# Optimization experiments

Measured on AMD Instinct MI355X. Metric: run time of the kernel, lower is better.

The kernel has to match this reference:

```python
import jax, jax.numpy as jnp
import numpy as np

N_A, N_P = 100000, 150000
N = N_A + N_P          # total nodes in concatenated feature matrix
D = 128                # emb_dim == hidden
C = 16                 # num_classes
E = 2000000            # nnz per relation


def setup_inputs() -> dict:
    key = jax.random.key(0)
    ks = jax.random.split(key, 16)
    s = 1.0 / np.sqrt(D)
    # coefficients as in init_coe: uniform(-b, b) then L1-normalized, coe_num = 1+2+2 = 5
    bound = np.sqrt(3.0 / 5)
    coe_np = np.random.RandomState(0).uniform(-bound, bound, 5)
    coe_np = coe_np / np.sum(np.abs(coe_np))
    return {
        "x0": jax.random.normal(ks[0], (N_A, D), jnp.float32),
        "x1": jax.random.normal(ks[1], (N_P, D), jnp.float32),
        "vals_ap": jax.random.uniform(ks[2], (E,), jnp.float32) * 0.01,
        "vals_pa": jax.random.uniform(ks[3], (E,), jnp.float32) * 0.01,
        # AP: rows are A nodes [0, N_A), cols are P nodes [N_A, N)
        "rows_ap": jax.random.randint(ks[4], (E,), 0, N_A, jnp.int32),
        "cols_ap": jax.random.randint(ks[5], (E,), N_A, N, jnp.int32),
        # PA: rows are P nodes [N_A, N), cols are A nodes [0, N_A)
        "rows_pa": jax.random.randint(ks[6], (E,), N_A, N, jnp.int32),
        "cols_pa": jax.random.randint(ks[7], (E,), 0, N_A, jnp.int32),
        "Wp0": jax.random.normal(ks[8], (D, D), jnp.float32) * s,
        "Wp1": jax.random.normal(ks[9], (D, D), jnp.float32) * s,
        "W1": jax.random.normal(ks[10], (D, D), jnp.float32) * s,
        "b1": jnp.zeros((D,), jnp.float32),
        "W2": jax.random.normal(ks[11], (D, C), jnp.float32) * s,
        "b2": jnp.zeros((C,), jnp.float32),
        "coe": jnp.asarray(coe_np, jnp.float32),
    }


def _spmm(rows, cols, vals, h):
    # sparse [N,N] @ dense [N,D] via gather + segment-sum
    return jax.ops.segment_sum(vals[:, None] * h[cols], rows, num_segments=N)


def _normalize(x):
    mean = x.mean(axis=1, keepdims=True)
    std = jnp.std(x, axis=1, keepdims=True, ddof=1)  # torch std is unbiased
    z = (x - mean) / std
    return jnp.where(jnp.isnan(z), 0.0, z)


def _power_pass(x, coe, ap, pa, first_order):
    # first_order: tuple of relation names in hop-1 order ("AP","PA") or ("PA","AP")
    rel = {"AP": ap, "PA": pa}
    res = coe[0] * x
    h = {}
    for ci, r in enumerate(first_order):
        h[r] = _spmm(*rel[r], x)
        res = res + coe[1 + ci] * h[r]
    # hop 2: compose relation j[:2] with previous result j[2:]
    second = [r + first_order[1 - i] for i, r in enumerate(first_order)]
    for ci, j in enumerate(second):
        out = _spmm(*rel[j[:2]], h[j[2:]])
        res = res + coe[3 + ci] * out
    return res


def reference(x0, x1, vals_ap, vals_pa, rows_ap, cols_ap, rows_pa, cols_pa,
              Wp0, Wp1, W1, b1, W2, b2, coe):
    ap = (rows_ap, cols_ap, vals_ap)
    pa = (rows_pa, cols_pa, vals_pa)
    # per-type projection then concat along node axis
    x = jnp.concatenate([x0 @ Wp0, x1 @ Wp1], axis=0)  # [N, D]
    x = jax.nn.relu(x @ W1 + b1)
    x = _normalize(x)
    # pass 1: lis = {1: [AP, PA], 2: [APPA, PAAP]}
    x = _power_pass(x, coe, ap, pa, ("AP", "PA"))
    # pass 2 (transposed series): lis_t = {1: [PA, AP], 2: [PAAP, APPA]}
    res = _power_pass(x, coe, ap, pa, ("PA", "AP"))
    return res @ W2 + b2  # [N, C]
```

## Files before the change

### kernel.cpp

```cpp
#include <hip/hip_runtime.h>
#include <hip/hip_bf16.h>


typedef float f32x2 __attribute__((ext_vector_type(2)));
typedef float f32x4 __attribute__((ext_vector_type(4)));
typedef short bf16x8 __attribute__((ext_vector_type(8)));

__device__ inline unsigned short f2bf(float x) {
    unsigned b = __float_as_uint(x);
    unsigned r = (b + 0x7fffu + ((b >> 16) & 1u)) >> 16;
    return (unsigned short)r;
}
__device__ inline float bflo(unsigned u) { return __uint_as_float(u << 16); }
__device__ inline float bfhi(unsigned u) { return __uint_as_float(u & 0xffff0000u); }

__device__ inline unsigned pk_fp8x4(float a, float b, float c, float d) {
    int v = __builtin_amdgcn_cvt_pk_fp8_f32(a, b, 0, false);
    v = __builtin_amdgcn_cvt_pk_fp8_f32(c, d, v, true);
    return (unsigned)v;
}

__global__ __launch_bounds__(128) void fuse_w(const float* __restrict__ Wp0,
                                              const float* __restrict__ Wp1,
                                              const float* __restrict__ W1,
                                              unsigned short* __restrict__ Mt0,
                                              unsigned short* __restrict__ Mt1) {
    int m = blockIdx.x >> 7;
    int i = blockIdx.x & 127;
    const float* Wp = m ? Wp1 : Wp0;
    unsigned short* Mt = m ? Mt1 : Mt0;
    __shared__ float r[128];
    int t = threadIdx.x;
    r[t] = Wp[i * 128 + t];
    __syncthreads();
    float acc = 0.f;
    #pragma unroll 8
    for (int k = 0; k < 128; ++k) acc += r[k] * W1[k * 128 + t];
    Mt[t * 128 + i] = f2bf(acc);
}

__global__ __launch_bounds__(256) void gemm_relu_norm(const float* __restrict__ xin,
                                                      const unsigned short* __restrict__ Mt,
                                                      const float* __restrict__ b1,
                                                      unsigned short* __restrict__ xbf,
                                                      unsigned char* __restrict__ x8,
                                                      int nrows) {
    __shared__ char xsh[64 * 256];
    __shared__ char xsl[64 * 256];
    __shared__ char mts[128 * 256];
    int t = threadIdx.x;
    long row0 = (long)blockIdx.x * 64;
    int rows_this = nrows - (int)row0;
    if (rows_this > 64) rows_this = 64;

    #pragma unroll
    for (int it = 0; it < 4; ++it) {
        int idx = it * 256 + t;
        int row = idx >> 4, slot = idx & 15;
        float4 v0 = {0.f, 0.f, 0.f, 0.f}, v1 = {0.f, 0.f, 0.f, 0.f};
        if (row < rows_this) {
            v0 = *(const float4*)(xin + (row0 + row) * 128 + slot * 8);
            v1 = *(const float4*)(xin + (row0 + row) * 128 + slot * 8 + 4);
        }
        float vv[8] = {v0.x, v0.y, v0.z, v0.w, v1.x, v1.y, v1.z, v1.w};
        unsigned hw[8], lw[8];
        #pragma unroll
        for (int j = 0; j < 8; ++j) {
            unsigned h = f2bf(vv[j]);
            float hv = __uint_as_float(h << 16);
            hw[j] = h;
            lw[j] = f2bf(vv[j] - hv);
        }
        uint4 ph, pl;
        ph.x = hw[0] | (hw[1] << 16); ph.y = hw[2] | (hw[3] << 16);
        ph.z = hw[4] | (hw[5] << 16); ph.w = hw[6] | (hw[7] << 16);
        pl.x = lw[0] | (lw[1] << 16); pl.y = lw[2] | (lw[3] << 16);
        pl.z = lw[4] | (lw[5] << 16); pl.w = lw[6] | (lw[7] << 16);
        int off = row * 256 + ((slot ^ (row & 7)) << 4);
        *(uint4*)&xsh[off] = ph;
        *(uint4*)&xsl[off] = pl;
    }
    #pragma unroll
    for (int it = 0; it < 8; ++it) {
        int idx = it * 256 + t;
        int row = idx >> 4, slot = idx & 15;
        uint4 mv = ((const uint4*)Mt)[idx];
        *(uint4*)&mts[row * 256 + ((slot ^ (row & 7)) << 4)] = mv;
    }
    __syncthreads();

    int w = t >> 6;
    int lidx = t & 15;
    int grp = (t >> 4) & 3;
    f32x4 acc[8];
    #pragma unroll
    for (int nt = 0; nt < 8; ++nt) acc[nt] = (f32x4){0.f, 0.f, 0.f, 0.f};

    #pragma unroll
    for (int ks = 0; ks < 4; ++ks) {
        int arow = w * 16 + lidx;
        int slot = ks * 4 + grp;
        bf16x8 ah = *(bf16x8*)&xsh[arow * 256 + ((slot ^ (arow & 7)) << 4)];
        bf16x8 al = *(bf16x8*)&xsl[arow * 256 + ((slot ^ (arow & 7)) << 4)];
        #pragma unroll
        for (int nt = 0; nt < 8; ++nt) {
            int brow = nt * 16 + lidx;
            bf16x8 bb = *(bf16x8*)&mts[brow * 256 + ((slot ^ (brow & 7)) << 4)];
            acc[nt] = __builtin_amdgcn_mfma_f32_16x16x32_bf16(al, bb, acc[nt], 0, 0, 0);
            acc[nt] = __builtin_amdgcn_mfma_f32_16x16x32_bf16(ah, bb, acc[nt], 0, 0, 0);
        }
    }

    float bias[8];
    #pragma unroll
    for (int nt = 0; nt < 8; ++nt) bias[nt] = b1[nt * 16 + lidx];

    #pragma unroll
    for (int r = 0; r < 4; ++r) {
        int row_loc = w * 16 + grp * 4 + r;
        float v[8];
        float s = 0.f;
        #pragma unroll
        for (int nt = 0; nt < 8; ++nt) {
            float x = acc[nt][r] + bias[nt];
            x = x > 0.f ? x : 0.f;
            v[nt] = x;
            s += x;
        }
        s += __shfl_xor(s, 1); s += __shfl_xor(s, 2);
        s += __shfl_xor(s, 4); s += __shfl_xor(s, 8);
        float mean = s * (1.0f / 128.0f);
        float q = 0.f;
        #pragma unroll
        for (int nt = 0; nt < 8; ++nt) {
            float d = v[nt] - mean;
            v[nt] = d;
            q += d * d;
        }
        q += __shfl_xor(q, 1); q += __shfl_xor(q, 2);
        q += __shfl_xor(q, 4); q += __shfl_xor(q, 8);
        float inv = 0.f;
        if (q > 0.f) inv = 1.0f / sqrtf(q * (1.0f / 127.0f));
        #pragma unroll
        for (int nt = 0; nt < 8; ++nt)
            *(unsigned short*)&xsh[row_loc * 256 + (nt * 16 + lidx) * 2] = f2bf(v[nt] * inv);
    }
    __syncthreads();

    #pragma unroll
    for (int it = 0; it < 4; ++it) {
        int idx = it * 256 + t;
        int row = idx >> 4, slot = idx & 15;
        if (row < rows_this) {
            uint4 zv = *(uint4*)&xsh[row * 256 + slot * 16];
            *(uint4*)(xbf + (row0 + row) * 128 + slot * 8) = zv;
            uint2 p8;
            p8.x = pk_fp8x4(bflo(zv.x), bfhi(zv.x), bflo(zv.y), bfhi(zv.y));
            p8.y = pk_fp8x4(bflo(zv.z), bfhi(zv.z), bflo(zv.w), bfhi(zv.w));
            *(uint2*)(x8 + (row0 + row) * 128 + slot * 8) = p8;
        }
    }
}

__global__ __launch_bounds__(256) void count_rows(const int* __restrict__ rows, int E,
                                                  int* __restrict__ cnt) {
    int i = (blockIdx.x * 256 + threadIdx.x) * 4;
    if (i + 4 <= E) {
        int4 r = *(const int4*)(rows + i);
        atomicAdd(&cnt[r.x], 1);
        atomicAdd(&cnt[r.y], 1);
        atomicAdd(&cnt[r.z], 1);
        atomicAdd(&cnt[r.w], 1);
    } else {
        for (; i < E; ++i) atomicAdd(&cnt[rows[i]], 1);
    }
}

__global__ __launch_bounds__(256) void scan1(const int* __restrict__ cnt, int R,
                                             int* __restrict__ rp, int* __restrict__ bt) {
    __shared__ int lds[256];
    int t = threadIdx.x, b = blockIdx.x;
    int base = b * 4096 + t * 16;
    int v[16];
    int s = 0;
    #pragma unroll
    for (int i = 0; i < 16; ++i) {
        int idx = base + i;
        int c = (idx < R) ? cnt[idx] : 0;
        v[i] = s;
        s += c;
    }
    lds[t] = s;
    __syncthreads();
    for (int off = 1; off < 256; off <<= 1) {
        int x = (t >= off) ? lds[t - off] : 0;
        __syncthreads();
        lds[t] += x;
        __syncthreads();
    }
    int excl = lds[t] - s;
    #pragma unroll
    for (int i = 0; i < 16; ++i) {
        int idx = base + i;
        if (idx < R) rp[idx] = excl + v[i];
    }
    if (t == 0) bt[b] = lds[255];
}

__global__ __launch_bounds__(64) void scan2(const int* __restrict__ bt, int B,
                                            int* __restrict__ bo, int* __restrict__ rp,
                                            int R, int E2) {
    int t = threadIdx.x;
    int v = (t < B) ? bt[t] : 0;
    int inc = v;
    #pragma unroll
    for (int off = 1; off < 64; off <<= 1) {
        int y = __shfl_up(inc, off);
        if (t >= off) inc += y;
    }
    if (t < B) bo[t] = inc - v;
    if (t == 0) rp[R] = E2;
}

__global__ __launch_bounds__(256) void scan3(int* __restrict__ rp, const int* __restrict__ bo,
                                             int R) {
    int i = blockIdx.x * 256 + threadIdx.x;
    if (i < R) rp[i] = rp[i] + bo[i >> 12];
}

__global__ __launch_bounds__(256) void binit(const int* __restrict__ rp, int NR,
                                             int nbuck, int* __restrict__ bcur) {
    int b = blockIdx.x * 256 + threadIdx.x;
    if (b < nbuck) {
        int r = b << 9;
        if (r > NR) r = NR;
        bcur[b] = rp[r];
    }
}

__global__ __launch_bounds__(256) void dhist(const int* __restrict__ rp, int R,
                                             int* __restrict__ dcnt) {
    __shared__ int h[64];
    int t = threadIdx.x;
    if (t < 64) h[t] = 0;
    __syncthreads();
    int i = blockIdx.x * 256 + t;
    if (i < R) {
        int d = rp[i + 1] - rp[i];
        if (d > 63) d = 63;
        atomicAdd(&h[d], 1);
    }
    __syncthreads();
    if (t < 64 && h[t]) atomicAdd(&dcnt[t], h[t]);
}

__global__ __launch_bounds__(64) void dscan(int* __restrict__ dcnt) {
    int t = threadIdx.x;
    int v = dcnt[t];
    int inc = v;
    #pragma unroll
    for (int off = 1; off < 64; off <<= 1) {
        int y = __shfl_up(inc, off);
        if (t >= off) inc += y;
    }
    dcnt[t] = inc - v;
}

__global__ __launch_bounds__(256) void dscatter(const int* __restrict__ rp, int R,
                                                int* __restrict__ dcur,
                                                int* __restrict__ order) {
    __shared__ int h[64], gb[64], c2[64];
    int t = threadIdx.x;
    if (t < 64) { h[t] = 0; c2[t] = 0; }
    __syncthreads();
    int i = blockIdx.x * 256 + t;
    int d = 0;
    if (i < R) {
        d = rp[i + 1] - rp[i];
        if (d > 63) d = 63;
        atomicAdd(&h[d], 1);
    }
    __syncthreads();
    if (t < 64) gb[t] = h[t] ? atomicAdd(&dcur[t], h[t]) : 0;
    __syncthreads();
    if (i < R) {
        int r = atomicAdd(&c2[d], 1);
        order[gb[d] + r] = i;
    }
}

__global__ __launch_bounds__(256) void partition_edges(const int* __restrict__ rows,
                                                       const int* __restrict__ cols,
                                                       const float* __restrict__ vals,
                                                       int E, int nbuck,
                                                       int* __restrict__ bcur,
                                                       int2* __restrict__ tmp) {
    __shared__ int hist[512];
    __shared__ int gbase[512];
    __shared__ int cnt2[512];
    int t = threadIdx.x;
    for (int b = t; b < nbuck; b += 256) { hist[b] = 0; cnt2[b] = 0; }
    __syncthreads();
    long base = (long)blockIdx.x * 4096;
    #pragma unroll
    for (int k = 0; k < 16; ++k) {
        long i = base + k * 256 + t;
        if (i < E) atomicAdd(&hist[rows[i] >> 9], 1);
    }
    __syncthreads();
    for (int b = t; b < nbuck; b += 256) {
        int h = hist[b];
        gbase[b] = h ? atomicAdd(&bcur[b], h) : 0;
    }
    __syncthreads();
    #pragma unroll
    for (int k = 0; k < 16; ++k) {
        long i = base + k * 256 + t;
        if (i < E) {
            int rl = rows[i];
            int b = rl >> 9;
            int rank = atomicAdd(&cnt2[b], 1);
            int2 rec;
            rec.x = ((rl - (b << 9)) << 18) | cols[i];
            rec.y = __float_as_int(vals[i]);
            tmp[gbase[b] + rank] = rec;
        }
    }
}

__global__ __launch_bounds__(1024) void place_edges(const int* __restrict__ rp,
                                                    const int2* __restrict__ tmp,
                                                    int NR,
                                                    int2* __restrict__ scv) {
    __shared__ int hist[512];
    __shared__ int hoff[512];
    int b = blockIdx.x;
    int srow = b << 9;
    int erow = srow + 512;
    if (erow > NR) erow = NR;
    int start = rp[srow], endp = rp[erow];
    int t = threadIdx.x;
    if (t < 512) hist[t] = 0;
    __syncthreads();

    for (int i = start + t; i < endp; i += 1024)
        atomicAdd(&hist[tmp[i].x >> 18], 1);
    __syncthreads();

    if (t < 512) hoff[t] = hist[t];
    __syncthreads();
    for (int off = 1; off < 512; off <<= 1) {
        int v = 0;
        if (t < 512 && t >= off) v = hoff[t - off];
        __syncthreads();
        if (t < 512) hoff[t] += v;
        __syncthreads();
    }
    if (t < 512) hoff[t] = start + hoff[t] - hist[t];
    __syncthreads();

    int i = start + t;
    for (; i + 3 * 1024 < endp; i += 4 * 1024) {
        int2 a0 = tmp[i];
        int2 a1 = tmp[i + 1024];
        int2 a2 = tmp[i + 2048];
        int2 a3 = tmp[i + 3072];
        int p0 = atomicAdd(&hoff[a0.x >> 18], 1);
        int p1 = atomicAdd(&hoff[a1.x >> 18], 1);
        int p2 = atomicAdd(&hoff[a2.x >> 18], 1);
        int p3 = atomicAdd(&hoff[a3.x >> 18], 1);
        int2 o0; o0.x = a0.x & 0x3ffff; o0.y = a0.y;
        int2 o1; o1.x = a1.x & 0x3ffff; o1.y = a1.y;
        int2 o2; o2.x = a2.x & 0x3ffff; o2.y = a2.y;
        int2 o3; o3.x = a3.x & 0x3ffff; o3.y = a3.y;
        scv[p0] = o0;
        scv[p1] = o1;
        scv[p2] = o2;
        scv[p3] = o3;
    }
    for (; i < endp; i += 1024) {
        int2 rec = tmp[i];
        int p = atomicAdd(&hoff[rec.x >> 18], 1);
        int2 o;
        o.x = rec.x & 0x3ffff;
        o.y = rec.y;
        scv[p] = o;
    }
}

#define DEC_FMA(qq, vv) do {                                                        \
    f32x2 vp_ = {(vv), (vv)};                                                       \
    acc[0] = __builtin_elementwise_fma(vp_, __builtin_amdgcn_cvt_pk_f32_fp8((qq).x, false), acc[0]); \
    acc[1] = __builtin_elementwise_fma(vp_, __builtin_amdgcn_cvt_pk_f32_fp8((qq).x, true),  acc[1]); \
    acc[2] = __builtin_elementwise_fma(vp_, __builtin_amdgcn_cvt_pk_f32_fp8((qq).y, false), acc[2]); \
    acc[3] = __builtin_elementwise_fma(vp_, __builtin_amdgcn_cvt_pk_f32_fp8((qq).y, true),  acc[3]); \
} while (0)

__device__ inline void spmm_core8(const int* __restrict__ rp,
                                  const int2* __restrict__ scv,
                                  const unsigned char* __restrict__ g8,
                                  int row, int f, f32x2* acc) {
    int beg = rp[row], end = rp[row + 1];
    int j = beg;
    if ((j & 1) && j < end) {
        int2 r0 = scv[j];
        uint2 q0 = *(const uint2*)(g8 + ((long)r0.x << 7) + f);
        float v0 = __int_as_float(r0.y);
        DEC_FMA(q0, v0);
        ++j;
    }
    for (; j + 8 <= end; j += 8) {
        int4 s01 = *(const int4*)(scv + j);
        int4 s23 = *(const int4*)(scv + j + 2);
        int4 s45 = *(const int4*)(scv + j + 4);
        int4 s67 = *(const int4*)(scv + j + 6);
        uint2 q0 = *(const uint2*)(g8 + ((long)s01.x << 7) + f);
        uint2 q1 = *(const uint2*)(g8 + ((long)s01.z << 7) + f);
        uint2 q2 = *(const uint2*)(g8 + ((long)s23.x << 7) + f);
        uint2 q3 = *(const uint2*)(g8 + ((long)s23.z << 7) + f);
        uint2 q4 = *(const uint2*)(g8 + ((long)s45.x << 7) + f);
        uint2 q5 = *(const uint2*)(g8 + ((long)s45.z << 7) + f);
        uint2 q6 = *(const uint2*)(g8 + ((long)s67.x << 7) + f);
        uint2 q7 = *(const uint2*)(g8 + ((long)s67.z << 7) + f);
        DEC_FMA(q0, __int_as_float(s01.y));
        DEC_FMA(q1, __int_as_float(s01.w));
        DEC_FMA(q2, __int_as_float(s23.y));
        DEC_FMA(q3, __int_as_float(s23.w));
        DEC_FMA(q4, __int_as_float(s45.y));
        DEC_FMA(q5, __int_as_float(s45.w));
        DEC_FMA(q6, __int_as_float(s67.y));
        DEC_FMA(q7, __int_as_float(s67.w));
    }
    for (; j + 2 <= end; j += 2) {
        int4 s01 = *(const int4*)(scv + j);
        uint2 q0 = *(const uint2*)(g8 + ((long)s01.x << 7) + f);
        uint2 q1 = *(const uint2*)(g8 + ((long)s01.z << 7) + f);
        DEC_FMA(q0, __int_as_float(s01.y));
        DEC_FMA(q1, __int_as_float(s01.w));
    }
    if (j < end) {
        int2 r0 = scv[j];
        uint2 q0 = *(const uint2*)(g8 + ((long)r0.x << 7) + f);
        float v0 = __int_as_float(r0.y);
        DEC_FMA(q0, v0);
    }
}

__global__ __launch_bounds__(256) void spmm_plain(const int* __restrict__ rp,
                                                  const int2* __restrict__ scv,
                                                  const unsigned char* __restrict__ x8,
                                                  const int* __restrict__ order,
                                                  unsigned short* __restrict__ houtbf,
                                                  unsigned char* __restrict__ hout8,
                                                  int R) {
    int qi = blockIdx.x * 16 + (threadIdx.x >> 4);
    if (qi >= R) return;
    int row = order[qi];
    int lane = threadIdx.x & 63;
    int f = (lane & 15) << 3;
    f32x2 acc[4];
    #pragma unroll
    for (int i = 0; i < 4; ++i) acc[i] = (f32x2){0.f, 0.f};
    spmm_core8(rp, scv, x8, row, f, acc);
    long o = ((long)row << 7) + f;
    uint4 ob;
    ob.x = (unsigned)f2bf(acc[0].x) | ((unsigned)f2bf(acc[0].y) << 16);
    ob.y = (unsigned)f2bf(acc[1].x) | ((unsigned)f2bf(acc[1].y) << 16);
    ob.z = (unsigned)f2bf(acc[2].x) | ((unsigned)f2bf(acc[2].y) << 16);
    ob.w = (unsigned)f2bf(acc[3].x) | ((unsigned)f2bf(acc[3].y) << 16);
    *(uint4*)(houtbf + o) = ob;
    uint2 o8;
    o8.x = pk_fp8x4(acc[0].x, acc[0].y, acc[1].x, acc[1].y);
    o8.y = pk_fp8x4(acc[2].x, acc[2].y, acc[3].x, acc[3].y);
    *(uint2*)(hout8 + o) = o8;
}

__global__ __launch_bounds__(256) void spmm_update(const int* __restrict__ rp,
                                                   const int2* __restrict__ scv,
                                                   const unsigned char* __restrict__ h8,
                                                   const unsigned short* __restrict__ hbf,
                                                   const int* __restrict__ order,
                                                   unsigned short* __restrict__ Xbf,
                                                   unsigned char* __restrict__ X8,
                                                   const float* __restrict__ coe,
                                                   int ihA, int iaA, int ihP, int iaP,
                                                   int NA, int R) {
    int qi = blockIdx.x * 16 + (threadIdx.x >> 4);
    if (qi >= R) return;
    int row = order[qi];
    int lane = threadIdx.x & 63;
    int f = (lane & 15) << 3;
    f32x2 acc[4];
    #pragma unroll
    for (int i = 0; i < 4; ++i) acc[i] = (f32x2){0.f, 0.f};
    spmm_core8(rp, scv, h8, row, f, acc);

    float c0 = coe[0];
    float ch = coe[row < NA ? ihA : ihP];
    float ca = coe[row < NA ? iaA : iaP];
    long o = ((long)row << 7) + f;
    uint4 xv = *(const uint4*)(Xbf + o);
    uint4 hs = *(const uint4*)(hbf + o);
    float r[8];
    r[0] = c0 * bflo(xv.x) + ch * bflo(hs.x) + ca * acc[0].x;
    r[1] = c0 * bfhi(xv.x) + ch * bfhi(hs.x) + ca * acc[0].y;
    r[2] = c0 * bflo(xv.y) + ch * bflo(hs.y) + ca * acc[1].x;
    r[3] = c0 * bfhi(xv.y) + ch * bfhi(hs.y) + ca * acc[1].y;
    r[4] = c0 * bflo(xv.z) + ch * bflo(hs.z) + ca * acc[2].x;
    r[5] = c0 * bfhi(xv.z) + ch * bfhi(hs.z) + ca * acc[2].y;
    r[6] = c0 * bflo(xv.w) + ch * bflo(hs.w) + ca * acc[3].x;
    r[7] = c0 * bfhi(xv.w) + ch * bfhi(hs.w) + ca * acc[3].y;
    uint4 ob;
    ob.x = (unsigned)f2bf(r[0]) | ((unsigned)f2bf(r[1]) << 16);
    ob.y = (unsigned)f2bf(r[2]) | ((unsigned)f2bf(r[3]) << 16);
    ob.z = (unsigned)f2bf(r[4]) | ((unsigned)f2bf(r[5]) << 16);
    ob.w = (unsigned)f2bf(r[6]) | ((unsigned)f2bf(r[7]) << 16);
    *(uint4*)(Xbf + o) = ob;
    uint2 o8;
    o8.x = pk_fp8x4(r[0], r[1], r[2], r[3]);
    o8.y = pk_fp8x4(r[4], r[5], r[6], r[7]);
    *(uint2*)(X8 + o) = o8;
}

__global__ __launch_bounds__(256) void spmm_update_out(const int* __restrict__ rp,
                                                       const int2* __restrict__ scv,
                                                       const unsigned char* __restrict__ h8,
                                                       const unsigned short* __restrict__ hbf,
                                                       const unsigned short* __restrict__ Xbf,
                                                       const int* __restrict__ order,
                                                       const float* __restrict__ coe,
                                                       const float* __restrict__ W2,
                                                       const float* __restrict__ b2,
                                                       float* __restrict__ out,
                                                       int ihA, int iaA, int ihP, int iaP,
                                                       int NA, int R) {
    __shared__ float xs[16 * 132];
    __shared__ float wT[16 * 132];
    __shared__ float bs[16];
    int t = threadIdx.x;
    #pragma unroll
    for (int i = 0; i < 8; ++i) {
        int idx = i * 256 + t;
        wT[(idx & 15) * 132 + (idx >> 4)] = W2[idx];
    }
    if (t < 16) bs[t] = b2[t];

    int rl = t >> 4;
    int qi = blockIdx.x * 16 + rl;
    int lane = t & 63;
    int f = (lane & 15) << 3;
    if (qi < R) {
        int row = order[qi];
        f32x2 acc[4];
        #pragma unroll
        for (int i = 0; i < 4; ++i) acc[i] = (f32x2){0.f, 0.f};
        spmm_core8(rp, scv, h8, row, f, acc);
        float c0 = coe[0];
        float ch = coe[row < NA ? ihA : ihP];
        float ca = coe[row < NA ? iaA : iaP];
        long o = ((long)row << 7) + f;
        uint4 xv = *(const uint4*)(Xbf + o);
        uint4 hs = *(const uint4*)(hbf + o);
        float* x = &xs[rl * 132 + f];
        x[0] = c0 * bflo(xv.x) + ch * bflo(hs.x) + ca * acc[0].x;
        x[1] = c0 * bfhi(xv.x) + ch * bfhi(hs.x) + ca * acc[0].y;
        x[2] = c0 * bflo(xv.y) + ch * bflo(hs.y) + ca * acc[1].x;
        x[3] = c0 * bfhi(xv.y) + ch * bfhi(hs.y) + ca * acc[1].y;
        x[4] = c0 * bflo(xv.z) + ch * bflo(hs.z) + ca * acc[2].x;
        x[5] = c0 * bfhi(xv.z) + ch * bfhi(hs.z) + ca * acc[2].y;
        x[6] = c0 * bflo(xv.w) + ch * bflo(hs.w) + ca * acc[3].x;
        x[7] = c0 * bfhi(xv.w) + ch * bfhi(hs.w) + ca * acc[3].y;
    }
    __syncthreads();
    int orl = t >> 4, c = t & 15;
    int oqi = blockIdx.x * 16 + orl;
    if (oqi < R) {
        long orow = order[oqi];
        const float* xrow = &xs[orl * 132];
        const float* wrow = &wT[c * 132];
        f32x4 a4 = {0.f, 0.f, 0.f, 0.f};
        #pragma unroll 8
        for (int k = 0; k < 128; k += 4) {
            f32x4 xv = *(const f32x4*)(xrow + k);
            f32x4 wv = *(const f32x4*)(wrow + k);
            a4 = __builtin_elementwise_fma(xv, wv, a4);
        }
        out[orow * 16 + c] = a4.x + a4.y + a4.z + a4.w + bs[c];
    }
}

extern "C" void kernel_launch(void* const* d_in, const int* in_sizes, int n_in,
                              void* d_out, int out_size, void* d_ws, size_t ws_size,
                              hipStream_t stream) {
    const float* x0  = (const float*)d_in[0];
    const float* x1  = (const float*)d_in[1];
    const float* vap = (const float*)d_in[2];
    const float* vpa = (const float*)d_in[3];
    const int*   rap = (const int*)d_in[4];
    const int*   cap = (const int*)d_in[5];
    const int*   rpa = (const int*)d_in[6];
    const int*   cpa = (const int*)d_in[7];
    const float* Wp0 = (const float*)d_in[8];
    const float* Wp1 = (const float*)d_in[9];
    const float* W1  = (const float*)d_in[10];
    const float* b1  = (const float*)d_in[11];
    const float* W2  = (const float*)d_in[12];
    const float* b2  = (const float*)d_in[13];
    const float* coe = (const float*)d_in[14];
    float* out = (float*)d_out;

    const int NA = in_sizes[0] / 128;
    const int NP = in_sizes[1] / 128;
    const int N  = NA + NP;
    const int E  = in_sizes[2];
    const int E2 = 2 * E;

    char* p = (char*)d_ws;
    auto alloc = [&](size_t bytes) {
        char* r = p;
        p += (bytes + 255) & ~(size_t)255;
        return r;
    };
    unsigned short* Xbf = (unsigned short*)alloc((size_t)N * 128 * 2);
    unsigned short* hbf = (unsigned short*)alloc((size_t)N * 128 * 2);
    unsigned char* X8 = (unsigned char*)alloc((size_t)N * 128);
    unsigned char* h8 = (unsigned char*)alloc((size_t)N * 128);
    unsigned short* Mt0 = (unsigned short*)alloc(128 * 128 * 2);
    unsigned short* Mt1 = (unsigned short*)alloc(128 * 128 * 2);
    int* cnt   = (int*)alloc((size_t)N * 4);
    int* rp    = (int*)alloc((size_t)(N + 1) * 4);
    int* order = (int*)alloc((size_t)N * 4);
    int* dcnt  = (int*)alloc(64 * 4);
    int* bt    = (int*)alloc(64 * 4);
    int* bo    = (int*)alloc(64 * 4);
    int2* scv  = (int2*)alloc(((size_t)E2 + 8) * 8);
    int* bcur  = (int*)alloc(512 * 4);
    if ((size_t)(p - (char*)d_ws) > ws_size) return;

    int2* tmp = (int2*)Xbf;

    const int nbuck = (N + 511) >> 9;
    const int pg = (E + 4095) / 4096;
    const int ng = (N + 255) / 256;

    hipMemsetAsync(cnt, 0, (size_t)N * 4, stream);
    hipMemsetAsync(dcnt, 0, 64 * 4, stream);
    hipMemsetAsync(scv + E2, 0, 8 * sizeof(int2), stream);
    const int cg = (E / 4 + 255) / 256;
    count_rows<<<cg, 256, 0, stream>>>(rap, E, cnt);
    count_rows<<<cg, 256, 0, stream>>>(rpa, E, cnt);
    int B = (N + 4095) / 4096;
    scan1<<<B, 256, 0, stream>>>(cnt, N, rp, bt);
    scan2<<<1, 64, 0, stream>>>(bt, B, bo, rp, N, E2);
    scan3<<<ng, 256, 0, stream>>>(rp, bo, N);
    binit<<<2, 256, 0, stream>>>(rp, N, nbuck, bcur);

    dhist<<<ng, 256, 0, stream>>>(rp, N, dcnt);
    dscan<<<1, 64, 0, stream>>>(dcnt);
    dscatter<<<ng, 256, 0, stream>>>(rp, N, dcnt, order);

    partition_edges<<<pg, 256, 0, stream>>>(rap, cap, vap, E, nbuck, bcur, tmp);
    partition_edges<<<pg, 256, 0, stream>>>(rpa, cpa, vpa, E, nbuck, bcur, tmp);
    place_edges<<<nbuck, 1024, 0, stream>>>(rp, tmp, N, scv);

    fuse_w<<<256, 128, 0, stream>>>(Wp0, Wp1, W1, Mt0, Mt1);
    gemm_relu_norm<<<(NA + 63) / 64, 256, 0, stream>>>(x0, Mt0, b1, Xbf, X8, NA);
    gemm_relu_norm<<<(NP + 63) / 64, 256, 0, stream>>>(
        x1, Mt1, b1, Xbf + (size_t)NA * 128, X8 + (size_t)NA * 128, NP);

    const int sg = (N + 15) / 16;

    spmm_plain<<<sg, 256, 0, stream>>>(rp, scv, X8, order, hbf, h8, N);
    spmm_update<<<sg, 256, 0, stream>>>(rp, scv, h8, hbf, order, Xbf, X8, coe,
                                        1, 3, 2, 4, NA, N);

    spmm_plain<<<sg, 256, 0, stream>>>(rp, scv, X8, order, hbf, h8, N);
    spmm_update_out<<<sg, 256, 0, stream>>>(rp, scv, h8, hbf, Xbf, order, coe,
                                            W2, b2, out, 2, 4, 1, 3, NA, N);
}
```

Measured before the change: 978.5 us.

## Replace global degree sort with per-window local degree ordering in one kernel

Three kernels (global degree histogram, scan, scatter) plus a memset are replaced by a single kernel that sorts rows by degree only within 1024-row windows, using a shared-memory histogram and a wave scan. This removes kernel launches and global atomics from the preprocessing phase. In exchange, row ordering is only locally balanced, so SpMM waves may see less uniform degree grouping across the whole graph, which could affect load balance in the SpMM kernels.

Result: faster. 937.7 us (-4.2%).

```diff
diff --git a/kernel.cpp b/kernel.cpp
--- a/kernel.cpp
+++ b/kernel.cpp
@@ -238,54 +238,46 @@
     }
 }
 
-__global__ __launch_bounds__(256) void dhist(const int* __restrict__ rp, int R,
-                                             int* __restrict__ dcnt) {
-    __shared__ int h[64];
+__global__ __launch_bounds__(256) void worder(const int* __restrict__ rp, int R,
+                                              int* __restrict__ order) {
+    __shared__ int h[64], base[64], c2[64];
     int t = threadIdx.x;
-    if (t < 64) h[t] = 0;
-    __syncthreads();
-    int i = blockIdx.x * 256 + t;
-    if (i < R) {
-        int d = rp[i + 1] - rp[i];
-        if (d > 63) d = 63;
-        atomicAdd(&h[d], 1);
-    }
-    __syncthreads();
-    if (t < 64 && h[t]) atomicAdd(&dcnt[t], h[t]);
-}
-
-__global__ __launch_bounds__(64) void dscan(int* __restrict__ dcnt) {
-    int t = threadIdx.x;
-    int v = dcnt[t];
-    int inc = v;
-    #pragma unroll
-    for (int off = 1; off < 64; off <<= 1) {
-        int y = __shfl_up(inc, off);
-        if (t >= off) inc += y;
-    }
-    dcnt[t] = inc - v;
-}
-
-__global__ __launch_bounds__(256) void dscatter(const int* __restrict__ rp, int R,
-                                                int* __restrict__ dcur,
-                                                int* __restrict__ order) {
-    __shared__ int h[64], gb[64], c2[64];
-    int t = threadIdx.x;
+    int w0 = blockIdx.x << 10;
+    int wend = w0 + 1024;
+    if (wend > R) wend = R;
     if (t < 64) { h[t] = 0; c2[t] = 0; }
     __syncthreads();
-    int i = blockIdx.x * 256 + t;
-    int d = 0;
-    if (i < R) {
-        d = rp[i + 1] - rp[i];
-        if (d > 63) d = 63;
-        atomicAdd(&h[d], 1);
-    }
-    __syncthreads();
-    if (t < 64) gb[t] = h[t] ? atomicAdd(&dcur[t], h[t]) : 0;
-    __syncthreads();
-    if (i < R) {
-        int r = atomicAdd(&c2[d], 1);
-        order[gb[d] + r] = i;
+    int d[4];
+    #pragma unroll
+    for (int k = 0; k < 4; ++k) {
+        int i = w0 + k * 256 + t;
+        int dd = 0;
+        if (i < wend) {
+            dd = rp[i + 1] - rp[i];
+            if (dd > 63) dd = 63;
+            atomicAdd(&h[dd], 1);
+        }
+        d[k] = dd;
+    }
+    __syncthreads();
+    if (t < 64) {
+        int v = h[t];
+        int inc = v;
+        #pragma unroll
+        for (int off = 1; off < 64; off <<= 1) {
+            int y = __shfl_up(inc, off);
+            if (t >= off) inc += y;
+        }
+        base[t] = inc - v;
+    }
+    __syncthreads();
+    #pragma unroll
+    for (int k = 0; k < 4; ++k) {
+        int i = w0 + k * 256 + t;
+        if (i < wend) {
+            int r = atomicAdd(&c2[d[k]], 1);
+            order[w0 + base[d[k]] + r] = i;
+        }
     }
 }
 
@@ -630,7 +622,6 @@
     int* cnt   = (int*)alloc((size_t)N * 4);
     int* rp    = (int*)alloc((size_t)(N + 1) * 4);
     int* order = (int*)alloc((size_t)N * 4);
-    int* dcnt  = (int*)alloc(64 * 4);
     int* bt    = (int*)alloc(64 * 4);
     int* bo    = (int*)alloc(64 * 4);
     int2* scv  = (int2*)alloc(((size_t)E2 + 8) * 8);
@@ -644,7 +635,6 @@
     const int ng = (N + 255) / 256;
 
     hipMemsetAsync(cnt, 0, (size_t)N * 4, stream);
-    hipMemsetAsync(dcnt, 0, 64 * 4, stream);
     hipMemsetAsync(scv + E2, 0, 8 * sizeof(int2), stream);
     const int cg = (E / 4 + 255) / 256;
     count_rows<<<cg, 256, 0, stream>>>(rap, E, cnt);
@@ -655,9 +645,7 @@
     scan3<<<ng, 256, 0, stream>>>(rp, bo, N);
     binit<<<2, 256, 0, stream>>>(rp, N, nbuck, bcur);
 
-    dhist<<<ng, 256, 0, stream>>>(rp, N, dcnt);
-    dscan<<<1, 64, 0, stream>>>(dcnt);
-    dscatter<<<ng, 256, 0, stream>>>(rp, N, dcnt, order);
+    worder<<<(N + 1023) / 1024, 256, 0, stream>>>(rp, N, order);
 
     partition_edges<<<pg, 256, 0, stream>>>(rap, cap, vap, E, nbuck, bcur, tmp);
     partition_edges<<<pg, 256, 0, stream>>>(rpa, cpa, vpa, E, nbuck, bcur, tmp);
```
